# Kernel optimization log

Hardware: AMD Instinct MI355X
Metric: run time of the kernel (lower is better)

Reference implementation:

```python
import jax, jax.numpy as jnp
import numpy as np

D_MODEL = 1024
N_HEAD = 16
HEAD_DIM = D_MODEL // N_HEAD

def setup_inputs() -> dict:
    key = jax.random.key(0)
    k1, k2, k3 = jax.random.split(key, 3)
    x = jax.random.normal(k1, (2, 2048, D_MODEL), dtype=jnp.float32)
    # torch Linear weights: [out_features, in_features]; scale like default init
    w_in = jax.random.normal(k2, (3 * D_MODEL, D_MODEL), dtype=jnp.float32) * (1.0 / np.sqrt(D_MODEL))
    w_out = jax.random.normal(k3, (D_MODEL, D_MODEL), dtype=jnp.float32) * (1.0 / np.sqrt(D_MODEL))
    return {"x": x, "w_in": w_in, "w_out": w_out}

def reference(x, w_in, w_out):
    B, T, D = x.shape
    qkv = jnp.einsum('btd,ed->bte', x, w_in)  # [B,T,3D]
    q, k, v = jnp.split(qkv, 3, axis=2)
    def heads(t):
        return t.reshape(B, T, N_HEAD, HEAD_DIM).transpose(0, 2, 1, 3)  # [B,H,T,hd]
    q, k, v = heads(q), heads(k), heads(v)
    att = jnp.einsum('bhqd,bhkd->bhqk', q, k) / np.sqrt(HEAD_DIM).astype(np.float32)
    # NOTE: original uses .tril() (zeroing, NOT -inf) before softmax — faithful reproduction
    causal = jnp.tril(jnp.ones((T, T), dtype=bool))
    att = jnp.where(causal, att, 0.0)
    att = jax.nn.softmax(att, axis=-1)
    out = jnp.einsum('bhqk,bhkd->bhqd', att, v)
    out = out.transpose(0, 2, 1, 3).reshape(B, T, D)
    return jnp.einsum('btd,ed->bte', out, w_out)
```

## Files before the change

kernel.cpp:

```cpp
#include <hip/hip_runtime.h>
#include <hip/hip_bf16.h>
#include <stdint.h>

#define TSEQ   2048
#define DMODEL 1024
#define NHEAD  16
#define HDIM   64

typedef __attribute__((ext_vector_type(8))) __bf16 bf16x8;
typedef __attribute__((ext_vector_type(4))) float f32x4;
typedef __attribute__((ext_vector_type(8))) unsigned short u16x8;

#define SC_LOG2E 0.18033688011112042f

#if __has_builtin(__builtin_amdgcn_exp2f)
#define EXP2F(x) __builtin_amdgcn_exp2f(x)
#else
#define EXP2F(x) __expf(0.6931471805599453f * (x))
#endif

__device__ __forceinline__ unsigned short f2bf(float f) {
    __hip_bfloat16 h = __float2bfloat16(f);
    return __builtin_bit_cast(unsigned short, h);
}
__device__ __forceinline__ float bf2f(unsigned short u) {
    union { unsigned int i; float f; } v;
    v.i = ((unsigned int)u) << 16;
    return v.f;
}

__device__ __forceinline__ void gld_lds16(const void* g, void* s) {
    __builtin_amdgcn_global_load_lds(
        (__attribute__((address_space(1))) void*)(void*)g,
        (__attribute__((address_space(3))) void*)s, 16, 0, 0);
}

#define NX4  (4096 * 1024 / 4)
#define NWI4 (3072 * 1024 / 4)
#define NWO4 (1024 * 1024 / 4)
__global__ void cast3_kernel(const float* __restrict__ x,
                             const float* __restrict__ wi,
                             const float* __restrict__ wo,
                             unsigned short* __restrict__ ox,
                             unsigned short* __restrict__ owi,
                             unsigned short* __restrict__ owo) {
    int i = blockIdx.x * blockDim.x + threadIdx.x;
    const float* s;
    unsigned short* d;
    int off;
    if (i < NX4)              { s = x;  d = ox;  off = i; }
    else if (i < NX4 + NWI4)  { s = wi; d = owi; off = i - NX4; }
    else                      { s = wo; d = owo; off = i - NX4 - NWI4; }
    float4 v = ((const float4*)s)[off];
    ushort4 u;
    u.x = f2bf(v.x); u.y = f2bf(v.y); u.z = f2bf(v.z); u.w = f2bf(v.w);
    ((ushort4*)d)[off] = u;
}

template<bool STORE_F32>
__global__ __launch_bounds__(256, 2)
void gemm_bt(const unsigned short* __restrict__ A,
             const unsigned short* __restrict__ B,
             void* __restrict__ C, int M, int N, int K) {
    (void)M;
    __shared__ unsigned short As[128 * 32];
    __shared__ unsigned short Bs[128 * 32];
    const int tid = threadIdx.x;
    const int nb = N >> 7;
    const int bm = blockIdx.x / nb;
    const int bn = blockIdx.x % nb;
    const int w  = tid >> 6, l = tid & 63;
    const int wr = w >> 1,  wc = w & 1;
    const int lr = l & 15,  lg = l >> 4;

    f32x4 acc[4][4] = {};

    const unsigned short* Ab = A + (size_t)bm * 128 * K;
    const unsigned short* Bb = B + (size_t)bn * 128 * K;

    const int c0 = tid, c1 = tid + 256;
    const int ar0 = c0 >> 2, ak0 = (c0 & 3) * 8;
    const int ar1 = c1 >> 2, ak1 = (c1 & 3) * 8;

    for (int kt = 0; kt < K; kt += 32) {
        __syncthreads();
        gld_lds16(Ab + (size_t)ar0 * K + kt + ak0, As + c0 * 8);
        gld_lds16(Ab + (size_t)ar1 * K + kt + ak1, As + c1 * 8);
        gld_lds16(Bb + (size_t)ar0 * K + kt + ak0, Bs + c0 * 8);
        gld_lds16(Bb + (size_t)ar1 * K + kt + ak1, Bs + c1 * 8);
        __syncthreads();

        bf16x8 af[4], bfr[4];
#pragma unroll
        for (int i = 0; i < 4; i++)
            af[i] = *(const bf16x8*)(As + (wr * 64 + i * 16 + lr) * 32 + lg * 8);
#pragma unroll
        for (int i = 0; i < 4; i++)
            bfr[i] = *(const bf16x8*)(Bs + (wc * 64 + i * 16 + lr) * 32 + lg * 8);
#pragma unroll
        for (int mi = 0; mi < 4; mi++)
#pragma unroll
            for (int ni = 0; ni < 4; ni++)
                acc[mi][ni] = __builtin_amdgcn_mfma_f32_16x16x32_bf16(
                    af[mi], bfr[ni], acc[mi][ni], 0, 0, 0);
    }

    const int row0 = bm * 128 + wr * 64;
    const int col0 = bn * 128 + wc * 64;
    const float qsc = (!STORE_F32 && bn < 8) ? SC_LOG2E : 1.0f;
#pragma unroll
    for (int mi = 0; mi < 4; mi++)
#pragma unroll
        for (int ni = 0; ni < 4; ni++)
#pragma unroll
            for (int r = 0; r < 4; r++) {
                const int row = row0 + mi * 16 + lg * 4 + r;
                const int col = col0 + ni * 16 + lr;
                if (STORE_F32)
                    ((float*)C)[(size_t)row * N + col] = acc[mi][ni][r];
                else
                    ((unsigned short*)C)[(size_t)row * N + col] =
                        f2bf(acc[mi][ni][r] * qsc);
            }
}

__global__ __launch_bounds__(256)
void vtran_kernel(const unsigned short* __restrict__ qkv,
                  unsigned short* __restrict__ vtg,
                  float* __restrict__ ts) {
    __shared__ unsigned short T[64][72];
    const int bid = blockIdx.x;
    const int kb_ = bid & 31;
    const int bh  = bid >> 5;
    const int b = bh >> 4, h = bh & 15;
    const int tid = threadIdx.x;

    const int r = tid >> 2, cq = (tid & 3) * 16;
    const unsigned short* src =
        qkv + ((size_t)(b * TSEQ + kb_ * 64 + r)) * 3072 + 2048 + h * 64 + cq;
    u16x8 v0 = *(const u16x8*)src;
    u16x8 v1 = *(const u16x8*)(src + 8);
#pragma unroll
    for (int i = 0; i < 8; i++) T[r][cq + i] = v0[i];
#pragma unroll
    for (int i = 0; i < 8; i++) T[r][cq + 8 + i] = v1[i];
    __syncthreads();

    const int d = tid >> 2, kq = (tid & 3) * 16;
    u16x8 o0, o1;
#pragma unroll
    for (int i = 0; i < 8; i++) o0[i] = T[kq + i][d];
#pragma unroll
    for (int i = 0; i < 8; i++) o1[i] = T[kq + 8 + i][d];
    unsigned short* dst = vtg + ((size_t)bh * 64 + d) * TSEQ + kb_ * 64 + kq;
    *(u16x8*)dst = o0;
    *(u16x8*)(dst + 8) = o1;

    float ps = 0.f;
#pragma unroll
    for (int i = 0; i < 8; i++) ps += bf2f(o0[i]) + bf2f(o1[i]);
    ps += __shfl_xor(ps, 1);
    ps += __shfl_xor(ps, 2);
    if ((tid & 3) == 0)
        ts[((size_t)bh * 32 + kb_) * 64 + d] = ps;
}

__global__ void vsuf2_kernel(const float* __restrict__ ts,
                             float* __restrict__ tsuf) {
    const int bh = blockIdx.x, d = threadIdx.x;
    float acc = 0.f;
    for (int t = 31; t >= 0; --t) {
        tsuf[((size_t)bh * 32 + t) * 64 + d] = acc;
        acc += ts[((size_t)bh * 32 + t) * 64 + d];
    }
}

__global__ __launch_bounds__(256, 2)
void attn_kernel(const unsigned short* __restrict__ qkv,
                 const unsigned short* __restrict__ vtg,
                 const float* __restrict__ tsuf,
                 unsigned short* __restrict__ out) {
    __shared__ __attribute__((aligned(16))) unsigned short Ks[2][4096];
    __shared__ __attribute__((aligned(16))) unsigned short Vs[2][4096];
    __shared__ __attribute__((aligned(16))) unsigned short Pl[4][32 * 72];

    const int tid = threadIdx.x;
    const int w = tid >> 6, l = tid & 63, lr = l & 15, lg = l >> 4;
    const int bid = blockIdx.x;
    const int j  = bid >> 5;
    const int p  = (j < 8) ? j : 23 - j;
    const int bh = (bid & 7) * 4 + ((bid >> 3) & 3);
    const int b = bh >> 4, h = bh & 15;
    const int strip  = (w < 2) ? (31 - p) : p;
    const int lastkt = strip;
    const int ntiles = 32 - p;
    const size_t rowbase = (size_t)b * TSEQ;
    const int qrow0 = strip * 64 + (w & 1) * 32;

    bf16x8 qf[2][2];
#pragma unroll
    for (int mi = 0; mi < 2; mi++) {
        const unsigned short* qp =
            qkv + (rowbase + qrow0 + mi * 16 + lr) * 3072 + h * 64 + lg * 8;
        qf[mi][0] = *(const bf16x8*)qp;
        qf[mi][1] = *(const bf16x8*)(qp + 32);
    }

    const unsigned short* ksrc[2];
    const unsigned short* vsrc[2];
#pragma unroll
    for (int jj = 0; jj < 2; jj++) {
        const int d = tid + jj * 256;
        const int fr = (d >> 7) * 16 + (d & 15);
        const int cc = ((d >> 6) & 1) * 32 + ((d & 63) >> 4) * 8;
        ksrc[jj] = qkv + (rowbase + fr) * 3072 + 1024 + h * 64 + cc;
        vsrc[jj] = vtg + ((size_t)bh * 64 + fr) * TSEQ + cc;
    }

#define STAGE(kt_, bufi) do {                                      \
        const size_t ko_ = (size_t)(kt_) * 64 * 3072;              \
        const int vo_ = (kt_) * 64;                                \
        gld_lds16(ksrc[0] + ko_, &Ks[bufi][tid * 8]);              \
        gld_lds16(ksrc[1] + ko_, &Ks[bufi][tid * 8 + 2048]);       \
        gld_lds16(vsrc[0] + vo_, &Vs[bufi][tid * 8]);              \
        gld_lds16(vsrc[1] + vo_, &Vs[bufi][tid * 8 + 2048]);       \
    } while (0)

    f32x4 o[2][4] = {};
    float rsum[2][4] = {};
    unsigned short* pw = &Pl[w][0];

    STAGE(0, 0);
    __syncthreads();

    int cur = 0;
    for (int kt = 0; kt < ntiles; ++kt) {
        if (kt + 1 < ntiles) STAGE(kt + 1, cur ^ 1);

        if (kt <= lastkt) {
            const unsigned short* kc = Ks[cur];
            const unsigned short* vc = Vs[cur];

            bf16x8 kb[4][2];
#pragma unroll
            for (int f = 0; f < 4; f++) {
                kb[f][0] = *(const bf16x8*)(kc + ((f * 2 + 0) * 64 + l) * 8);
                kb[f][1] = *(const bf16x8*)(kc + ((f * 2 + 1) * 64 + l) * 8);
            }

            float pvv[2][4][4];
            __builtin_amdgcn_s_setprio(1);
#pragma unroll
            for (int mi = 0; mi < 2; mi++)
#pragma unroll
                for (int f = 0; f < 4; f++) {
                    f32x4 z = {0.f, 0.f, 0.f, 0.f};
                    f32x4 s = __builtin_amdgcn_mfma_f32_16x16x32_bf16(qf[mi][0], kb[f][0], z, 0, 0, 0);
                    s = __builtin_amdgcn_mfma_f32_16x16x32_bf16(qf[mi][1], kb[f][1], s, 0, 0, 0);
#pragma unroll
                    for (int r = 0; r < 4; r++) pvv[mi][f][r] = s[r];
                }
            __builtin_amdgcn_s_setprio(0);

            if (kt == lastkt) {
#pragma unroll
                for (int mi = 0; mi < 2; mi++)
#pragma unroll
                    for (int f = 0; f < 4; f++) {
                        const int kcol = kt * 64 + f * 16 + lr;
#pragma unroll
                        for (int r = 0; r < 4; r++) {
                            const int qr = qrow0 + mi * 16 + lg * 4 + r;
                            if (kcol > qr) pvv[mi][f][r] = 0.f;
                        }
                    }
            }

#pragma unroll
            for (int mi = 0; mi < 2; mi++)
#pragma unroll
                for (int f = 0; f < 4; f++)
#pragma unroll
                    for (int r = 0; r < 4; r++) {
                        float pp = EXP2F(pvv[mi][f][r]);
                        rsum[mi][r] += pp;
                        pw[(mi * 16 + lg * 4 + r) * 72 + f * 16 + lr] = f2bf(pp);
                    }

            bf16x8 pa[2][2];
#pragma unroll
            for (int mi = 0; mi < 2; mi++) {
                pa[mi][0] = *(const bf16x8*)(pw + (mi * 16 + lr) * 72 + lg * 8);
                pa[mi][1] = *(const bf16x8*)(pw + (mi * 16 + lr) * 72 + 32 + lg * 8);
            }
            bf16x8 vb[4][2];
#pragma unroll
            for (int f2 = 0; f2 < 4; f2++) {
                vb[f2][0] = *(const bf16x8*)(vc + ((f2 * 2 + 0) * 64 + l) * 8);
                vb[f2][1] = *(const bf16x8*)(vc + ((f2 * 2 + 1) * 64 + l) * 8);
            }
            __builtin_amdgcn_s_setprio(1);
#pragma unroll
            for (int mi = 0; mi < 2; mi++)
#pragma unroll
                for (int f2 = 0; f2 < 4; f2++) {
                    o[mi][f2] = __builtin_amdgcn_mfma_f32_16x16x32_bf16(pa[mi][0], vb[f2][0], o[mi][f2], 0, 0, 0);
                    o[mi][f2] = __builtin_amdgcn_mfma_f32_16x16x32_bf16(pa[mi][1], vb[f2][1], o[mi][f2], 0, 0, 0);
                }
            __builtin_amdgcn_s_setprio(0);
        }

        __syncthreads();
        cur ^= 1;
    }
#undef STAGE

#pragma unroll
    for (int d = 1; d < 16; d <<= 1)
#pragma unroll
        for (int mi = 0; mi < 2; mi++)
#pragma unroll
            for (int r = 0; r < 4; r++)
                rsum[mi][r] += __shfl_xor(rsum[mi][r], d);

    const float nmask = (float)((31 - lastkt) * 64);
    const float* tp = tsuf + ((size_t)bh * 32 + lastkt) * 64;
#pragma unroll
    for (int mi = 0; mi < 2; mi++)
#pragma unroll
        for (int r = 0; r < 4; r++) {
            const float inv = 1.f / (rsum[mi][r] + nmask);
#pragma unroll
            for (int f2 = 0; f2 < 4; f2++) {
                float num = o[mi][f2][r] + tp[f2 * 16 + lr];
                out[(rowbase + qrow0 + mi * 16 + lg * 4 + r) * 1024 + h * 64 + f2 * 16 + lr] =
                    f2bf(num * inv);
            }
        }
}

extern "C" void kernel_launch(void* const* d_in, const int* in_sizes, int n_in,
                              void* d_out, int out_size, void* d_ws, size_t ws_size,
                              hipStream_t stream) {
    const float* x     = (const float*)d_in[0];
    const float* w_in  = (const float*)d_in[1];
    const float* w_out = (const float*)d_in[2];

    unsigned short* ws  = (unsigned short*)d_ws;
    unsigned short* xb  = ws;
    unsigned short* wib = xb  + (size_t)4096 * 1024;
    unsigned short* wob = wib + (size_t)3072 * 1024;
    unsigned short* qkv = wob + (size_t)1024 * 1024;
    unsigned short* ao  = qkv + (size_t)4096 * 3072;
    float* tsuf = (float*)(ao + (size_t)4096 * 1024);
    unsigned short* vtg = (unsigned short*)(tsuf + 32 * 32 * 64);
    float* ts = (float*)(vtg + (size_t)32 * 64 * 2048);

    cast3_kernel<<<(NX4 + NWI4 + NWO4) / 256, 256, 0, stream>>>(
        x, w_in, w_out, xb, wib, wob);

    gemm_bt<false><<<(4096 / 128) * (3072 / 128), 256, 0, stream>>>(
        xb, wib, qkv, 4096, 3072, 1024);
    vtran_kernel<<<32 * 32, 256, 0, stream>>>(qkv, vtg, ts);
    vsuf2_kernel<<<32, 64, 0, stream>>>(ts, tsuf);
    attn_kernel<<<512, 256, 0, stream>>>(qkv, vtg, tsuf, ao);
    gemm_bt<true><<<(4096 / 128) * (1024 / 128), 256, 0, stream>>>(
        ao, wob, (float*)d_out, 4096, 1024, 1024);
}
```

Baseline: 117.0 us.

## Pair adjacent causal strips per block and compute softmax row sums via MFMA

Measured after the change: 116.4 us. About the same (-0.6%).

```diff
diff --git a/kernel.cpp b/kernel.cpp
--- a/kernel.cpp
+++ b/kernel.cpp
@@ -188,12 +188,12 @@
     const int w = tid >> 6, l = tid & 63, lr = l & 15, lg = l >> 4;
     const int bid = blockIdx.x;
     const int j  = bid >> 5;
-    const int p  = (j < 8) ? j : 23 - j;
+    const int s  = (j < 8) ? j : 23 - j;
     const int bh = (bid & 7) * 4 + ((bid >> 3) & 3);
     const int b = bh >> 4, h = bh & 15;
-    const int strip  = (w < 2) ? (31 - p) : p;
+    const int strip  = 2 * s + ((w < 2) ? 1 : 0);
     const int lastkt = strip;
-    const int ntiles = 32 - p;
+    const int ntiles = 2 * s + 2;
     const size_t rowbase = (size_t)b * TSEQ;
     const int qrow0 = strip * 64 + (w & 1) * 32;
 
@@ -205,6 +205,10 @@
         qf[mi][0] = *(const bf16x8*)qp;
         qf[mi][1] = *(const bf16x8*)(qp + 32);
     }
+
+    bf16x8 onesf;
+#pragma unroll
+    for (int i = 0; i < 8; i++) onesf[i] = (__bf16)1.0f;
 
     const unsigned short* ksrc[2];
     const unsigned short* vsrc[2];
@@ -227,7 +231,7 @@
     } while (0)
 
     f32x4 o[2][4] = {};
-    float rsum[2][4] = {};
+    f32x4 rs[2] = {};
     unsigned short* pw = &Pl[w][0];
 
     STAGE(0, 0);
@@ -255,10 +259,10 @@
 #pragma unroll
                 for (int f = 0; f < 4; f++) {
                     f32x4 z = {0.f, 0.f, 0.f, 0.f};
-                    f32x4 s = __builtin_amdgcn_mfma_f32_16x16x32_bf16(qf[mi][0], kb[f][0], z, 0, 0, 0);
-                    s = __builtin_amdgcn_mfma_f32_16x16x32_bf16(qf[mi][1], kb[f][1], s, 0, 0, 0);
-#pragma unroll
-                    for (int r = 0; r < 4; r++) pvv[mi][f][r] = s[r];
+                    f32x4 sv = __builtin_amdgcn_mfma_f32_16x16x32_bf16(qf[mi][0], kb[f][0], z, 0, 0, 0);
+                    sv = __builtin_amdgcn_mfma_f32_16x16x32_bf16(qf[mi][1], kb[f][1], sv, 0, 0, 0);
+#pragma unroll
+                    for (int r = 0; r < 4; r++) pvv[mi][f][r] = sv[r];
                 }
             __builtin_amdgcn_s_setprio(0);
 
@@ -283,7 +287,6 @@
 #pragma unroll
                     for (int r = 0; r < 4; r++) {
                         float pp = EXP2F(pvv[mi][f][r]);
-                        rsum[mi][r] += pp;
                         pw[(mi * 16 + lg * 4 + r) * 72 + f * 16 + lr] = f2bf(pp);
                     }
 
@@ -301,12 +304,15 @@
             }
             __builtin_amdgcn_s_setprio(1);
 #pragma unroll
-            for (int mi = 0; mi < 2; mi++)
+            for (int mi = 0; mi < 2; mi++) {
+                rs[mi] = __builtin_amdgcn_mfma_f32_16x16x32_bf16(pa[mi][0], onesf, rs[mi], 0, 0, 0);
+                rs[mi] = __builtin_amdgcn_mfma_f32_16x16x32_bf16(pa[mi][1], onesf, rs[mi], 0, 0, 0);
 #pragma unroll
                 for (int f2 = 0; f2 < 4; f2++) {
                     o[mi][f2] = __builtin_amdgcn_mfma_f32_16x16x32_bf16(pa[mi][0], vb[f2][0], o[mi][f2], 0, 0, 0);
                     o[mi][f2] = __builtin_amdgcn_mfma_f32_16x16x32_bf16(pa[mi][1], vb[f2][1], o[mi][f2], 0, 0, 0);
                 }
+            }
             __builtin_amdgcn_s_setprio(0);
         }
 
@@ -315,21 +321,13 @@
     }
 #undef STAGE
 
-#pragma unroll
-    for (int d = 1; d < 16; d <<= 1)
-#pragma unroll
-        for (int mi = 0; mi < 2; mi++)
-#pragma unroll
-            for (int r = 0; r < 4; r++)
-                rsum[mi][r] += __shfl_xor(rsum[mi][r], d);
-
     const float nmask = (float)((31 - lastkt) * 64);
     const float* tp = tsuf + ((size_t)bh * 32 + lastkt) * 64;
 #pragma unroll
     for (int mi = 0; mi < 2; mi++)
 #pragma unroll
         for (int r = 0; r < 4; r++) {
-            const float inv = 1.f / (rsum[mi][r] + nmask);
+            const float inv = 1.f / (rs[mi][r] + nmask);
 #pragma unroll
             for (int f2 = 0; f2 < 4; f2++) {
                 float num = o[mi][f2][r] + tp[f2 * 16 + lr];
```
